# Kernel optimization log

Measured on AMD Instinct MI355X. Metric: run time of the kernel, lower is better.

## Reference

```python
import jax, jax.numpy as jnp
import numpy as np

BLOCKS, LAYERS, KS = 4, 2, 2
DILATIONS = [2 ** i for _ in range(BLOCKS) for i in range(LAYERS)]  # [1,2]*4
B, C_IN, N, T = 16, 2, 2048, 12
RC, DC, SC, EC, OUT = 32, 32, 256, 512, 12
L = BLOCKS * LAYERS
BN_EPS = 1e-5


def setup_inputs() -> dict:
    key = jax.random.key(0)
    ks = jax.random.split(key, 24)
    # raw inputs
    x = jax.random.normal(ks[0], (B, C_IN, N, T), dtype=jnp.float32)
    # two fixed supports: row-normalized random adjacency (dense, as in GraphWaveNet transition matrices)
    A_raw = jax.random.uniform(ks[1], (2, N, N), dtype=jnp.float32)
    A = A_raw / jnp.sum(A_raw, axis=2, keepdims=True)
    nodevec1 = jax.random.normal(ks[2], (N, 10), dtype=jnp.float32)
    nodevec2 = jax.random.normal(ks[3], (10, N), dtype=jnp.float32)
    s = 0.1  # weight scale to keep activations in a sane range
    filter_w = jax.random.normal(ks[4], (L, DC, RC, KS), dtype=jnp.float32) * s
    filter_b = jax.random.normal(ks[5], (L, DC), dtype=jnp.float32) * s
    gate_w = jax.random.normal(ks[6], (L, DC, RC, KS), dtype=jnp.float32) * s
    gate_b = jax.random.normal(ks[7], (L, DC), dtype=jnp.float32) * s
    skip_w = jax.random.normal(ks[8], (L, SC, DC), dtype=jnp.float32) * s
    skip_b = jax.random.normal(ks[9], (L, SC), dtype=jnp.float32) * s
    gcn_w = jax.random.normal(ks[10], (L, RC, 7 * DC), dtype=jnp.float32) * s
    gcn_b = jax.random.normal(ks[11], (L, RC), dtype=jnp.float32) * s
    bn_gamma = 1.0 + 0.1 * jax.random.normal(ks[12], (L, RC), dtype=jnp.float32)
    bn_beta = 0.1 * jax.random.normal(ks[13], (L, RC), dtype=jnp.float32)
    bn_mean = 0.1 * jax.random.normal(ks[14], (L, RC), dtype=jnp.float32)
    bn_var = 1.0 + jax.random.uniform(ks[15], (L, RC), dtype=jnp.float32)
    start_w = jax.random.normal(ks[16], (RC, C_IN), dtype=jnp.float32) * s
    start_b = jax.random.normal(ks[17], (RC,), dtype=jnp.float32) * s
    end1_w = jax.random.normal(ks[18], (EC, SC), dtype=jnp.float32) * s
    end1_b = jax.random.normal(ks[19], (EC,), dtype=jnp.float32) * s
    end2_w = jax.random.normal(ks[20], (OUT, EC), dtype=jnp.float32) * s
    end2_b = jax.random.normal(ks[21], (OUT,), dtype=jnp.float32) * s
    return dict(x=x, A=A, nodevec1=nodevec1, nodevec2=nodevec2,
                filter_w=filter_w, filter_b=filter_b, gate_w=gate_w, gate_b=gate_b,
                skip_w=skip_w, skip_b=skip_b, gcn_w=gcn_w, gcn_b=gcn_b,
                bn_gamma=bn_gamma, bn_beta=bn_beta, bn_mean=bn_mean, bn_var=bn_var,
                start_w=start_w, start_b=start_b, end1_w=end1_w, end1_b=end1_b,
                end2_w=end2_w, end2_b=end2_b)


def _conv1x1(x, w, b):
    # x: [b,c,n,t], w: [o,c] -> [b,o,n,t]
    return jnp.einsum('oc,bcnt->bont', w, x) + b[None, :, None, None]


def _dilated_conv2(x, w, b, d):
    # kernel (1,2) with time dilation d; out length T-d (valid conv)
    xa, xb = x[..., :-d], x[..., d:]
    y = jnp.einsum('oc,bcnt->bont', w[:, :, 0], xa) + jnp.einsum('oc,bcnt->bont', w[:, :, 1], xb)
    return y + b[None, :, None, None]


def _fwd(x, A, nodevec1, nodevec2, filter_w, filter_b, gate_w, gate_b,
         skip_w, skip_b, gcn_w, gcn_b, bn_gamma, bn_beta, bn_mean, bn_var,
         start_w, start_b, end1_w, end1_b, end2_w, end2_b):
    # pad 1 step at the start of time; T becomes 13 == receptive_field
    x = jnp.pad(x, ((0, 0), (0, 0), (0, 0), (1, 0)))
    x = x[:, :2]
    x = _conv1x1(x, start_w, start_b)  # [B,RC,N,13]
    # adaptive adjacency
    adp = jax.nn.softmax(jax.nn.relu(nodevec1 @ nodevec2), axis=1)
    supports = [A[0], A[1], adp]
    skip = None
    for i, d in enumerate(DILATIONS):
        residual = x
        filt = jnp.tanh(_dilated_conv2(residual, filter_w[i], filter_b[i], d))
        gate = jax.nn.sigmoid(_dilated_conv2(residual, gate_w[i], gate_b[i], d))
        x = filt * gate  # [B,DC,N,T-d]
        s = _conv1x1(x, skip_w[i], skip_b[i])  # [B,SC,N,T']
        skip = s if skip is None else s + skip[..., -s.shape[3]:]
        # GCN: order-2 diffusion over 3 supports, concat, 1x1 mix (dropout is identity in eval)
        outs = [x]
        for a in supports:
            x1 = jnp.einsum('bcvt,vw->bcwt', x, a)
            x2 = jnp.einsum('bcvt,vw->bcwt', x1, a)
            outs.extend([x1, x2])
        h = jnp.concatenate(outs, axis=1)  # [B,7*DC,N,T']
        x = _conv1x1(h, gcn_w[i], gcn_b[i])
        x = x + residual[..., -x.shape[3]:]
        # BatchNorm2d in eval mode (running stats)
        inv = bn_gamma[i] / jnp.sqrt(bn_var[i] + BN_EPS)
        x = (x - bn_mean[i][None, :, None, None]) * inv[None, :, None, None] + bn_beta[i][None, :, None, None]
    x = jax.nn.relu(skip)
    x = jax.nn.relu(_conv1x1(x, end1_w, end1_b))
    x = _conv1x1(x, end2_w, end2_b)  # [B,OUT,N,1]
    return x


def reference(x, A, nodevec1, nodevec2, filter_w, filter_b, gate_w, gate_b,
              skip_w, skip_b, gcn_w, gcn_b, bn_gamma, bn_beta, bn_mean, bn_var,
              start_w, start_b, end1_w, end1_b, end2_w, end2_b):
    return _fwd(x, A, nodevec1, nodevec2, filter_w, filter_b, gate_w, gate_b,
                skip_w, skip_b, gcn_w, gcn_b, bn_gamma, bn_beta, bn_mean, bn_var,
                start_w, start_b, end1_w, end1_b, end2_w, end2_b)
```

## Files before the change

### kernel.cpp

```cpp
#include <hip/hip_runtime.h>
#include <math.h>


#define NNODE 2048
#define NLAYER 8
#define SSTR ((size_t)NNODE * NNODE)

typedef unsigned short u16;
typedef unsigned int u32;
typedef __attribute__((ext_vector_type(8))) short bf16x8;
typedef __attribute__((ext_vector_type(4))) float f32x4;

__device__ __forceinline__ u16 f2bf(float f) {
    unsigned u = __builtin_bit_cast(unsigned, f);
    u += 0x7fffu + ((u >> 16) & 1u);
    return (u16)(u >> 16);
}
__device__ __forceinline__ float bf2f(u16 h) {
    unsigned u = ((unsigned)h) << 16;
    return __builtin_bit_cast(float, u);
}
__device__ __forceinline__ float bflo(u32 p) { return __builtin_bit_cast(float, p << 16); }
__device__ __forceinline__ float bfhi(u32 p) { return __builtin_bit_cast(float, p & 0xffff0000u); }
__device__ __forceinline__ u32 pack2(float a, float b) {
    return (u32)f2bf(a) | ((u32)f2bf(b) << 16);
}

__device__ __forceinline__ void gld16(const void* g, void* l) {
    __builtin_amdgcn_global_load_lds(
        (const __attribute__((address_space(1))) unsigned int*)g,
        (__attribute__((address_space(3))) unsigned int*)l, 16, 0, 0);
}

__global__ __launch_bounds__(256) void k_adp_mm(const float* __restrict__ nv1,
                                                const float* __restrict__ nv2,
                                                float* __restrict__ P) {
    int v = blockIdx.y;
    int w = blockIdx.x * 256 + threadIdx.x;
    float acc = 0.f;
#pragma unroll
    for (int k = 0; k < 10; ++k) acc += nv1[v * 10 + k] * nv2[k * NNODE + w];
    P[(size_t)v * NNODE + w] = acc;
}

__global__ __launch_bounds__(256) void k_softmax(float* __restrict__ P) {
    int v = blockIdx.x, tid = threadIdx.x;
    float* row = P + (size_t)v * NNODE;
    float m = 0.f;
    for (int w = tid; w < NNODE; w += 256) m = fmaxf(m, fmaxf(row[w], 0.f));
#pragma unroll
    for (int off = 32; off > 0; off >>= 1) m = fmaxf(m, __shfl_down(m, off));
    __shared__ float redm[4];
    __shared__ float reds[4];
    int wave = tid >> 6, lane = tid & 63;
    if (lane == 0) redm[wave] = m;
    __syncthreads();
    m = fmaxf(fmaxf(redm[0], redm[1]), fmaxf(redm[2], redm[3]));
    float s = 0.f;
    for (int w = tid; w < NNODE; w += 256) s += expf(fmaxf(row[w], 0.f) - m);
#pragma unroll
    for (int off = 32; off > 0; off >>= 1) s += __shfl_down(s, off);
    if (lane == 0) reds[wave] = s;
    __syncthreads();
    s = reds[0] + reds[1] + reds[2] + reds[3];
    float inv = 1.f / s;
    for (int w = tid; w < NNODE; w += 256) row[w] = expf(fmaxf(row[w], 0.f) - m) * inv;
}

__global__ __launch_bounds__(256) void k_transp(const float* __restrict__ A,
                                                const float* __restrict__ adp,
                                                u16* __restrict__ ST,
                                                u16* __restrict__ Sbf) {
    __shared__ float tile[32][33];
    int s = blockIdx.z;
    const float* src = (s < 2) ? (A + (size_t)s * SSTR) : adp;
    int v0 = blockIdx.y * 32, w0 = blockIdx.x * 32;
    int tx = threadIdx.x & 31, ty = threadIdx.x >> 5;
    u16* dst2 = Sbf + (size_t)s * SSTR;
#pragma unroll
    for (int p = 0; p < 4; ++p) {
        float v = src[(size_t)(v0 + ty + p * 8) * NNODE + w0 + tx];
        tile[ty + p * 8][tx] = v;
        dst2[(size_t)(v0 + ty + p * 8) * NNODE + w0 + tx] = f2bf(v);
    }
    __syncthreads();
    u16* dst = ST + (size_t)(2 * s) * SSTR;
#pragma unroll
    for (int p = 0; p < 4; ++p)
        dst[(size_t)(w0 + ty + p * 8) * NNODE + v0 + tx] = f2bf(tile[tx][ty + p * 8]);
}

__global__ __launch_bounds__(256) void k_skprep(const float* __restrict__ skw,
                                                const float* __restrict__ skb,
                                                u16* __restrict__ skwB,
                                                float* __restrict__ skbsum) {
    int idx = blockIdx.x * 256 + threadIdx.x;
    int sc = idx >> 8, k = idx & 255, l = k >> 5, ci = k & 31;
    skwB[idx] = f2bf(skw[((size_t)l * 256 + sc) * 32 + ci]);
    if (blockIdx.x == 0) {
        float s = 0.f;
#pragma unroll
        for (int ll = 0; ll < 8; ++ll) s += skb[ll * 256 + threadIdx.x];
        skbsum[threadIdx.x] = s;
    }
}

__global__ __launch_bounds__(256) void k_gemm_mfma(
    const u16* __restrict__ A, int lda, size_t asstr,
    const u16* __restrict__ BT, size_t bsstr,
    u16* __restrict__ C, int ldc, size_t csstr, int sbase) {
    __shared__ u16 Asl[128 * 32];
    __shared__ u16 Bsl[128 * 32];
    const int tid = threadIdx.x;
    const int wave = tid >> 6, lane = tid & 63;
    const int sidx = sbase + blockIdx.z;
    const u16* Ab = A + sidx * asstr + (size_t)blockIdx.y * 128 * lda;
    const u16* Bb = BT + sidx * bsstr + (size_t)blockIdx.x * 128 * NNODE;
    const int tr = tid >> 2;
    const int tc = (tid & 3) * 8;
    char* AslB = (char*)Asl + wave * 1024;
    char* BslB = (char*)Bsl + wave * 1024;
    const int wm = (wave & 1) * 64, wn = (wave >> 1) * 64;
    const int fr = lane & 15;
    const int fk = (lane >> 4) * 8;
    f32x4 acc[4][4];
#pragma unroll
    for (int i = 0; i < 4; ++i)
#pragma unroll
        for (int j = 0; j < 4; ++j) acc[i][j] = (f32x4){0.f, 0.f, 0.f, 0.f};

    for (int k0 = 0; k0 < 2048; k0 += 32) {
        gld16(Ab + (size_t)tr * lda + k0 + tc, AslB);
        gld16(Ab + (size_t)(tr + 64) * lda + k0 + tc, AslB + 4096);
        gld16(Bb + (size_t)tr * NNODE + k0 + tc, BslB);
        gld16(Bb + (size_t)(tr + 64) * NNODE + k0 + tc, BslB + 4096);
        __syncthreads();
        bf16x8 af[4], bf[4];
#pragma unroll
        for (int i = 0; i < 4; ++i)
            af[i] = *(const bf16x8*)&Asl[(wm + i * 16 + fr) * 32 + fk];
#pragma unroll
        for (int j = 0; j < 4; ++j)
            bf[j] = *(const bf16x8*)&Bsl[(wn + j * 16 + fr) * 32 + fk];
#pragma unroll
        for (int i = 0; i < 4; ++i)
#pragma unroll
            for (int j = 0; j < 4; ++j)
                acc[i][j] = __builtin_amdgcn_mfma_f32_16x16x32_bf16(af[i], bf[j], acc[i][j], 0, 0, 0);
        __syncthreads();
    }
    u16* Cb = C + sidx * csstr + (size_t)(blockIdx.y * 128 + wm) * ldc + blockIdx.x * 128 + wn;
    const int orow = (lane >> 4) * 4;
#pragma unroll
    for (int i = 0; i < 4; ++i)
#pragma unroll
        for (int j = 0; j < 4; ++j)
#pragma unroll
            for (int r = 0; r < 4; ++r)
                Cb[(size_t)(i * 16 + orow + r) * ldc + j * 16 + fr] = f2bf(acc[i][j][r]);
}

__global__ __launch_bounds__(512, 2) void k_gemmZ(const u16* __restrict__ Xg,
                                                  const u16* __restrict__ ST,
                                                  u16* __restrict__ Z, int pass) {
    __shared__ __align__(16) char ldsb[131072];
    const int tid = threadIdx.x;
    const int wave = tid >> 6, lane = tid & 63;
    const int m0 = blockIdx.y * 256;
    const int slice = pass * 3 + (blockIdx.x >> 3);
    const int n0 = (blockIdx.x & 7) * 256;
    const u16* AbG = Xg + (size_t)m0 * 2048;
    const u16* BbG = ST + (size_t)slice * SSTR + (size_t)n0 * 2048;

    const int xorc = ((tid & 7) ^ ((tid >> 3) & 7)) << 3;
    const size_t aRow = (size_t)(tid >> 3) * 2048 + xorc;
    const int bRowLoc = ((tid >> 8) << 6) + (((tid >> 6) & 3) << 3) + ((tid >> 3) & 7);
    const size_t bRow = (size_t)bRowLoc * 2048 + xorc;
    const int aw = wave << 10;
    const int bw = ((wave >> 2) << 13) + ((wave & 3) << 10);

    const int fr = lane & 15;
    const int cl4 = lane >> 4;
    const int ch0 = (cl4 ^ (fr & 7)) << 4;
    const int ch1 = ch0 ^ 64;
    const int aRd = ((wave & 1) << 14) + fr * 128;
    const int bRd = ((wave >> 1) << 13) + fr * 128;
    const int wm = (wave & 1) << 7;
    const int wn = (wave >> 1) << 6;

    char* A0 = ldsb;
    char* A1 = ldsb + 32768;
    char* B0 = ldsb + 65536;
    char* B1 = ldsb + 98304;

    auto STA = [&](char* Abase, int k0, int q) {
        const size_t g = (size_t)(q << 6) * 2048 + aRow + k0;
        gld16(AbG + g, Abase + (q << 13) + aw);
        gld16(AbG + g + (size_t)128 * 2048, Abase + 16384 + (q << 13) + aw);
    };
    auto STB = [&](char* Bbase, int k0, int q) {
        const size_t g = (size_t)(q << 5) * 2048 + bRow + k0;
        gld16(BbG + g, Bbase + (q << 12) + bw);
        gld16(BbG + g + (size_t)128 * 2048, Bbase + 16384 + (q << 12) + bw);
    };

    f32x4 acc[8][4];
#pragma unroll
    for (int i = 0; i < 8; ++i)
#pragma unroll
        for (int j = 0; j < 4; ++j) acc[i][j] = (f32x4){0.f, 0.f, 0.f, 0.f};

    STA(A0, 0, 0); STA(A0, 0, 1); STB(B0, 0, 0); STB(B0, 0, 1);
    STA(A1, 64, 0); STB(B1, 64, 0); STB(B1, 64, 1);
    asm volatile("s_waitcnt vmcnt(6)" ::: "memory");
    asm volatile("s_barrier" ::: "memory");

    char *Ac = A0, *Ao = A1, *Bc = B0, *Bo = B1;
    bf16x8 af[4][2], bfl[2][2], bfh[2][2];

    for (int T = 0; T < 32; ++T) {
#pragma unroll
        for (int i = 0; i < 4; ++i) {
            af[i][0] = *(const bf16x8*)(Ac + aRd + (i << 11) + ch0);
            af[i][1] = *(const bf16x8*)(Ac + aRd + (i << 11) + ch1);
        }
#pragma unroll
        for (int j = 0; j < 2; ++j) {
            bfl[j][0] = *(const bf16x8*)(Bc + bRd + (j << 11) + ch0);
            bfl[j][1] = *(const bf16x8*)(Bc + bRd + (j << 11) + ch1);
        }
        if (T < 31) STA(Ao, (T + 1) * 64, 1);
        asm volatile("s_barrier" ::: "memory");
        asm volatile("s_waitcnt lgkmcnt(0)" ::: "memory");
        __builtin_amdgcn_sched_barrier(0);
        __builtin_amdgcn_s_setprio(1);
#pragma unroll
        for (int i = 0; i < 4; ++i)
#pragma unroll
            for (int j = 0; j < 2; ++j) {
                acc[i][j] = __builtin_amdgcn_mfma_f32_16x16x32_bf16(af[i][0], bfl[j][0], acc[i][j], 0, 0, 0);
                acc[i][j] = __builtin_amdgcn_mfma_f32_16x16x32_bf16(af[i][1], bfl[j][1], acc[i][j], 0, 0, 0);
            }
        __builtin_amdgcn_s_setprio(0);
#pragma unroll
        for (int j = 0; j < 2; ++j) {
            bfh[j][0] = *(const bf16x8*)(Bc + bRd + 4096 + (j << 11) + ch0);
            bfh[j][1] = *(const bf16x8*)(Bc + bRd + 4096 + (j << 11) + ch1);
        }
        asm volatile("s_barrier" ::: "memory");
        asm volatile("s_waitcnt lgkmcnt(0)" ::: "memory");
        __builtin_amdgcn_sched_barrier(0);
        __builtin_amdgcn_s_setprio(1);
#pragma unroll
        for (int i = 0; i < 4; ++i)
#pragma unroll
            for (int j = 0; j < 2; ++j) {
                acc[i][2 + j] = __builtin_amdgcn_mfma_f32_16x16x32_bf16(af[i][0], bfh[j][0], acc[i][2 + j], 0, 0, 0);
                acc[i][2 + j] = __builtin_amdgcn_mfma_f32_16x16x32_bf16(af[i][1], bfh[j][1], acc[i][2 + j], 0, 0, 0);
            }
        __builtin_amdgcn_s_setprio(0);
#pragma unroll
        for (int i = 0; i < 4; ++i) {
            af[i][0] = *(const bf16x8*)(Ac + aRd + 8192 + (i << 11) + ch0);
            af[i][1] = *(const bf16x8*)(Ac + aRd + 8192 + (i << 11) + ch1);
        }
        if (T < 30) { STA(Ac, (T + 2) * 64, 0); STB(Bc, (T + 2) * 64, 0); }
        asm volatile("s_barrier" ::: "memory");
        asm volatile("s_waitcnt lgkmcnt(0)" ::: "memory");
        __builtin_amdgcn_sched_barrier(0);
        __builtin_amdgcn_s_setprio(1);
#pragma unroll
        for (int i = 0; i < 4; ++i)
#pragma unroll
            for (int j = 0; j < 2; ++j) {
                acc[4 + i][2 + j] = __builtin_amdgcn_mfma_f32_16x16x32_bf16(af[i][0], bfh[j][0], acc[4 + i][2 + j], 0, 0, 0);
                acc[4 + i][2 + j] = __builtin_amdgcn_mfma_f32_16x16x32_bf16(af[i][1], bfh[j][1], acc[4 + i][2 + j], 0, 0, 0);
            }
        __builtin_amdgcn_s_setprio(0);
        if (T < 30) STB(Bc, (T + 2) * 64, 1);
        asm volatile("s_barrier" ::: "memory");
        __builtin_amdgcn_sched_barrier(0);
        __builtin_amdgcn_s_setprio(1);
#pragma unroll
        for (int i = 0; i < 4; ++i)
#pragma unroll
            for (int j = 0; j < 2; ++j) {
                acc[4 + i][j] = __builtin_amdgcn_mfma_f32_16x16x32_bf16(af[i][0], bfl[j][0], acc[4 + i][j], 0, 0, 0);
                acc[4 + i][j] = __builtin_amdgcn_mfma_f32_16x16x32_bf16(af[i][1], bfl[j][1], acc[4 + i][j], 0, 0, 0);
            }
        __builtin_amdgcn_s_setprio(0);
        if (T < 30) {
            asm volatile("s_waitcnt vmcnt(6)" ::: "memory");
        } else if (T == 30) {
            asm volatile("s_waitcnt vmcnt(0)" ::: "memory");
        }
        asm volatile("s_barrier" ::: "memory");
        char* t;
        t = Ac; Ac = Ao; Ao = t;
        t = Bc; Bc = Bo; Bo = t;
    }

    const int col0 = (blockIdx.x >> 3) * 2048 + (blockIdx.x & 7) * 256;
    u16* Cb = Z + (size_t)(m0 + wm) * 6144 + col0 + wn;
    const int orow = cl4 * 4;
#pragma unroll
    for (int i = 0; i < 8; ++i)
#pragma unroll
        for (int j = 0; j < 4; ++j)
#pragma unroll
            for (int r = 0; r < 4; ++r)
                Cb[(size_t)(i * 16 + orow + r) * 6144 + j * 16 + fr] = f2bf(acc[i][j][r]);
}

__global__ __launch_bounds__(256) void k_gemmZ128(const u16* __restrict__ Xg,
                                                  const u16* __restrict__ ST,
                                                  u16* __restrict__ Z, int pass) {
    __shared__ u16 Asl[2][128 * 32];
    __shared__ u16 Bsl[2][128 * 32];
    const int tid = threadIdx.x;
    const int wave = tid >> 6, lane = tid & 63;
    const int m0 = blockIdx.y * 128;
    const int slice = pass * 3 + (blockIdx.x >> 4);
    const int nIn = (blockIdx.x & 15) * 128;
    const u16* Ab = Xg + (size_t)m0 * 2048;
    const u16* Bb = ST + (size_t)slice * SSTR + (size_t)nIn * NNODE;
    const int tr = tid >> 2;
    const int tc = (tid & 3) * 8;
    char* AslB0 = (char*)Asl[0] + wave * 1024;
    char* AslB1 = (char*)Asl[1] + wave * 1024;
    char* BslB0 = (char*)Bsl[0] + wave * 1024;
    char* BslB1 = (char*)Bsl[1] + wave * 1024;
    const int wm = (wave & 1) * 64, wn = (wave >> 1) * 64;
    const int fr = lane & 15;
    const int fk = (lane >> 4) * 8;
    f32x4 acc[4][4];
#pragma unroll
    for (int i = 0; i < 4; ++i)
#pragma unroll
        for (int j = 0; j < 4; ++j) acc[i][j] = (f32x4){0.f, 0.f, 0.f, 0.f};

    for (int k0 = 0; k0 < 2048; k0 += 64) {
        gld16(Ab + (size_t)tr * 2048 + k0 + tc, AslB0);
        gld16(Ab + (size_t)(tr + 64) * 2048 + k0 + tc, AslB0 + 4096);
        gld16(Ab + (size_t)tr * 2048 + k0 + 32 + tc, AslB1);
        gld16(Ab + (size_t)(tr + 64) * 2048 + k0 + 32 + tc, AslB1 + 4096);
        gld16(Bb + (size_t)tr * NNODE + k0 + tc, BslB0);
        gld16(Bb + (size_t)(tr + 64) * NNODE + k0 + tc, BslB0 + 4096);
        gld16(Bb + (size_t)tr * NNODE + k0 + 32 + tc, BslB1);
        gld16(Bb + (size_t)(tr + 64) * NNODE + k0 + 32 + tc, BslB1 + 4096);
        __syncthreads();
#pragma unroll
        for (int h = 0; h < 2; ++h) {
            bf16x8 af[4], bf[4];
#pragma unroll
            for (int i = 0; i < 4; ++i)
                af[i] = *(const bf16x8*)&Asl[h][(wm + i * 16 + fr) * 32 + fk];
#pragma unroll
            for (int j = 0; j < 4; ++j)
                bf[j] = *(const bf16x8*)&Bsl[h][(wn + j * 16 + fr) * 32 + fk];
#pragma unroll
            for (int i = 0; i < 4; ++i)
#pragma unroll
                for (int j = 0; j < 4; ++j)
                    acc[i][j] = __builtin_amdgcn_mfma_f32_16x16x32_bf16(af[i], bf[j], acc[i][j], 0, 0, 0);
        }
        __syncthreads();
    }
    u16* Cb = Z + (size_t)(m0 + wm) * 6144 + blockIdx.x * 128 + wn;
    const int orow = (lane >> 4) * 4;
#pragma unroll
    for (int i = 0; i < 4; ++i)
#pragma unroll
        for (int j = 0; j < 4; ++j)
#pragma unroll
            for (int r = 0; r < 4; ++r)
                Cb[(size_t)(i * 16 + orow + r) * 6144 + j * 16 + fr] = f2bf(acc[i][j][r]);
}

__global__ __launch_bounds__(256) void k_start(const float* __restrict__ xin,
                                               const float* __restrict__ sw,
                                               const float* __restrict__ sb,
                                               u16* __restrict__ out, int b0) {
    int n = blockIdx.x * 256 + threadIdx.x;
    int t = blockIdx.y;
    int bl = blockIdx.z;
    int b = b0 + bl;
    float x0 = 0.f, x1 = 0.f;
    if (t > 0) {
        x0 = xin[((size_t)(b * 2 + 0) * NNODE + n) * 12 + (t - 1)];
        x1 = xin[((size_t)(b * 2 + 1) * NNODE + n) * 12 + (t - 1)];
    }
#pragma unroll
    for (int co = 0; co < 32; ++co) {
        float v = sw[co * 2 + 0] * x0 + sw[co * 2 + 1] * x1 + sb[co];
        out[((size_t)(bl * 32 + co) * 13 + t) * NNODE + n] = f2bf(v);
    }
}

__global__ __launch_bounds__(256) void k_gate(const u16* __restrict__ cur,
                                              u16* __restrict__ xg,
                                              u16* __restrict__ nxt,
                                              int T, int Tn, int d,
                                              const float* __restrict__ fw,
                                              const float* __restrict__ fb,
                                              const float* __restrict__ gw,
                                              const float* __restrict__ gb,
                                              const float* __restrict__ gcwl,
                                              const float* __restrict__ gcbl,
                                              u16* __restrict__ xl,
                                              int layer, int donxt) {
    __shared__ float4 wp[1024];
    __shared__ float w0[32][33];
    int tid = threadIdx.x;
#pragma unroll
    for (int u = 0; u < 4; ++u) {
        int idx = tid + u * 256;
        int ci = idx >> 5, co = idx & 31;
        wp[idx] = make_float4(fw[co * 64 + ci * 2], fw[co * 64 + ci * 2 + 1],
                              gw[co * 64 + ci * 2], gw[co * 64 + ci * 2 + 1]);
        w0[ci][co] = gcwl[co * 224 + ci];
    }
    __syncthreads();
    int n = blockIdx.x * 512 + tid * 2;
    int t = blockIdx.y;
    int bl = blockIdx.z;
    float f0[32], f1[32], g0[32], g1[32];
#pragma unroll
    for (int co = 0; co < 32; ++co) { f0[co] = 0.f; f1[co] = 0.f; g0[co] = 0.f; g1[co] = 0.f; }
    for (int ci = 0; ci < 32; ++ci) {
        size_t ba = ((size_t)(bl * 32 + ci) * T + t) * NNODE + n;
        size_t bb = ((size_t)(bl * 32 + ci) * T + t + d) * NNODE + n;
        u32 ua = *(const u32*)&cur[ba];
        u32 ub = *(const u32*)&cur[bb];
        float xa0 = bflo(ua), xa1 = bfhi(ua);
        float xb0 = bflo(ub), xb1 = bfhi(ub);
#pragma unroll
        for (int co = 0; co < 32; ++co) {
            float4 w = wp[ci * 32 + co];
            f0[co] += w.x * xa0 + w.y * xb0;
            f1[co] += w.x * xa1 + w.y * xb1;
            g0[co] += w.z * xa0 + w.w * xb0;
            g1[co] += w.z * xa1 + w.w * xb1;
        }
    }
#pragma unroll
    for (int co = 0; co < 32; ++co) {
        float fbv = fb[co], gbv = gb[co];
        float a0 = tanhf(f0[co] + fbv) * (1.f / (1.f + expf(-(g0[co] + gbv))));
        float a1 = tanhf(f1[co] + fbv) * (1.f / (1.f + expf(-(g1[co] + gbv))));
        f0[co] = a0; f1[co] = a1;
        size_t o = ((size_t)(bl * 32 + co) * Tn + t) * NNODE + n;
        *(u32*)&xg[o] = pack2(a0, a1);
    }
    if (t == Tn - 1) {
        size_t o2 = ((size_t)(bl * 2048 + n)) * 256 + layer * 32;
#pragma unroll
        for (int co = 0; co < 32; ++co) {
            xl[o2 + co] = f2bf(f0[co]);
            xl[o2 + 256 + co] = f2bf(f1[co]);
        }
    }
    if (donxt) {
#pragma unroll
        for (int cop = 0; cop < 32; ++cop) {
            float s0 = gcbl[cop], s1 = s0;
#pragma unroll
            for (int ci = 0; ci < 32; ++ci) {
                float wv = w0[ci][cop];
                s0 += wv * f0[ci];
                s1 += wv * f1[ci];
            }
            size_t o = ((size_t)(bl * 32 + cop) * Tn + t) * NNODE + n;
            *(u32*)&nxt[o] = pack2(s0, s1);
        }
    }
}

__global__ __launch_bounds__(256) void k_accum(const u16* __restrict__ Z,
                                               int cbase,
                                               const float* __restrict__ gcnw,
                                               u16* __restrict__ outp,
                                               const u16* __restrict__ resid,
                                               int Tn, int d, int finalf,
                                               const float* __restrict__ bng,
                                               const float* __restrict__ bnb,
                                               const float* __restrict__ bnm,
                                               const float* __restrict__ bnv) {
    __shared__ float wl[3][32][32];
    int tid = threadIdx.x;
    for (int u = tid; u < 3072; u += 256) {
        int g = u >> 10, ci = (u >> 5) & 31, co = u & 31;
        wl[g][ci][co] = gcnw[co * 224 + cbase + g * 32 + ci];
    }
    __syncthreads();
    int n = blockIdx.x * 512 + tid * 2;
    int t = blockIdx.y, bl = blockIdx.z;
    float a0[32], a1[32];
#pragma unroll
    for (int co = 0; co < 32; ++co) { a0[co] = 0.f; a1[co] = 0.f; }
    for (int ci = 0; ci < 32; ++ci) {
        size_t m = (size_t)(bl * 32 + ci) * Tn + t;
#pragma unroll
        for (int g = 0; g < 3; ++g) {
            u32 zz = *(const u32*)&Z[m * 6144 + g * 2048 + n];
            float v0 = bflo(zz), v1 = bfhi(zz);
#pragma unroll
            for (int cq = 0; cq < 8; ++cq) {
                float4 w = *(const float4*)&wl[g][ci][cq * 4];
                a0[cq * 4 + 0] += w.x * v0; a1[cq * 4 + 0] += w.x * v1;
                a0[cq * 4 + 1] += w.y * v0; a1[cq * 4 + 1] += w.y * v1;
                a0[cq * 4 + 2] += w.z * v0; a1[cq * 4 + 2] += w.z * v1;
                a0[cq * 4 + 3] += w.w * v0; a1[cq * 4 + 3] += w.w * v1;
            }
        }
    }
#pragma unroll
    for (int co = 0; co < 32; ++co) {
        size_t o = ((size_t)(bl * 32 + co) * Tn + t) * NNODE + n;
        u32 oo = *(const u32*)&outp[o];
        float v0 = bflo(oo) + a0[co];
        float v1 = bfhi(oo) + a1[co];
        if (finalf) {
            size_t ro = ((size_t)(bl * 32 + co) * (Tn + d) + t + d) * NNODE + n;
            u32 rr = *(const u32*)&resid[ro];
            v0 += bflo(rr); v1 += bfhi(rr);
            float inv = bng[co] * rsqrtf(bnv[co] + 1e-5f);
            float mu = bnm[co], be = bnb[co];
            v0 = (v0 - mu) * inv + be;
            v1 = (v1 - mu) * inv + be;
        }
        *(u32*)&outp[o] = pack2(v0, v1);
    }
}

__global__ __launch_bounds__(256) void k_cast(const float* __restrict__ src,
                                              u16* __restrict__ dst) {
    int i = blockIdx.x * 256 + threadIdx.x;
    dst[i] = f2bf(src[i]);
}

__global__ __launch_bounds__(256) void k_skipg(const u16* __restrict__ xl,
                                               const u16* __restrict__ skwB,
                                               const float* __restrict__ skbsum,
                                               u16* __restrict__ skipT) {
    __shared__ u16 Asl[128 * 32];
    __shared__ u16 Bsl[128 * 32];
    const int tid = threadIdx.x;
    const int wave = tid >> 6, lane = tid & 63;
    const int m0 = blockIdx.y * 128;
    const int n0 = blockIdx.x * 128;
    const int tr = tid >> 2;
    const int tc = (tid & 3) * 8;
    char* AslB = (char*)Asl + wave * 1024;
    char* BslB = (char*)Bsl + wave * 1024;
    const int wm = (wave & 1) * 64, wn = (wave >> 1) * 64;
    const int fr = lane & 15;
    const int fk = (lane >> 4) * 8;
    const u16* Ab = xl + (size_t)m0 * 256;
    const u16* Bb = skwB + (size_t)n0 * 256;
    f32x4 acc[4][4];
#pragma unroll
    for (int i = 0; i < 4; ++i)
#pragma unroll
        for (int j = 0; j < 4; ++j) acc[i][j] = (f32x4){0.f, 0.f, 0.f, 0.f};
    for (int k0 = 0; k0 < 256; k0 += 32) {
        gld16(Ab + (size_t)tr * 256 + k0 + tc, AslB);
        gld16(Ab + (size_t)(tr + 64) * 256 + k0 + tc, AslB + 4096);
        gld16(Bb + (size_t)tr * 256 + k0 + tc, BslB);
        gld16(Bb + (size_t)(tr + 64) * 256 + k0 + tc, BslB + 4096);
        __syncthreads();
        bf16x8 af[4], bf[4];
#pragma unroll
        for (int i = 0; i < 4; ++i)
            af[i] = *(const bf16x8*)&Asl[(wm + i * 16 + fr) * 32 + fk];
#pragma unroll
        for (int j = 0; j < 4; ++j)
            bf[j] = *(const bf16x8*)&Bsl[(wn + j * 16 + fr) * 32 + fk];
#pragma unroll
        for (int i = 0; i < 4; ++i)
#pragma unroll
            for (int j = 0; j < 4; ++j)
                acc[i][j] = __builtin_amdgcn_mfma_f32_16x16x32_bf16(af[i], bf[j], acc[i][j], 0, 0, 0);
        __syncthreads();
    }
    const int orow = (lane >> 4) * 4;
#pragma unroll
    for (int i = 0; i < 4; ++i)
#pragma unroll
        for (int r = 0; r < 4; ++r) {
            int m = m0 + wm + i * 16 + orow + r;
            size_t ob = (size_t)m * 256 + n0 + wn;
#pragma unroll
            for (int j = 0; j < 4; ++j) {
                int col = n0 + wn + j * 16 + fr;
                skipT[ob + j * 16 + fr] = f2bf(fmaxf(acc[i][j][r] + skbsum[col], 0.f));
            }
        }
}

__global__ __launch_bounds__(256) void k_end1m(const u16* __restrict__ E1,
                                               const u16* __restrict__ skT,
                                               const float* __restrict__ bias,
                                               u16* __restrict__ h) {
    __shared__ u16 Asl[128 * 32];
    __shared__ u16 Bsl[128 * 32];
    const int tid = threadIdx.x;
    const int wave = tid >> 6, lane = tid & 63;
    const int b = blockIdx.z;
    const int m0 = blockIdx.y * 128;
    const int n0 = blockIdx.x * 128;
    const int tr = tid >> 2;
    const int tc = (tid & 3) * 8;
    char* AslB = (char*)Asl + wave * 1024;
    char* BslB = (char*)Bsl + wave * 1024;
    const int wm = (wave & 1) * 64, wn = (wave >> 1) * 64;
    const int fr = lane & 15;
    const int fk = (lane >> 4) * 8;
    const u16* Ab = E1 + (size_t)m0 * 256;
    const u16* Bb = skT + ((size_t)b * NNODE + n0) * 256;
    f32x4 acc[4][4];
#pragma unroll
    for (int i = 0; i < 4; ++i)
#pragma unroll
        for (int j = 0; j < 4; ++j) acc[i][j] = (f32x4){0.f, 0.f, 0.f, 0.f};
    for (int k0 = 0; k0 < 256; k0 += 32) {
        gld16(Ab + (size_t)tr * 256 + k0 + tc, AslB);
        gld16(Ab + (size_t)(tr + 64) * 256 + k0 + tc, AslB + 4096);
        gld16(Bb + (size_t)tr * 256 + k0 + tc, BslB);
        gld16(Bb + (size_t)(tr + 64) * 256 + k0 + tc, BslB + 4096);
        __syncthreads();
        bf16x8 af[4], bf[4];
#pragma unroll
        for (int i = 0; i < 4; ++i)
            af[i] = *(const bf16x8*)&Asl[(wm + i * 16 + fr) * 32 + fk];
#pragma unroll
        for (int j = 0; j < 4; ++j)
            bf[j] = *(const bf16x8*)&Bsl[(wn + j * 16 + fr) * 32 + fk];
#pragma unroll
        for (int i = 0; i < 4; ++i)
#pragma unroll
            for (int j = 0; j < 4; ++j)
                acc[i][j] = __builtin_amdgcn_mfma_f32_16x16x32_bf16(af[i], bf[j], acc[i][j], 0, 0, 0);
        __syncthreads();
    }
    const int orow = (lane >> 4) * 4;
#pragma unroll
    for (int i = 0; i < 4; ++i)
#pragma unroll
        for (int r = 0; r < 4; ++r) {
            int m = m0 + wm + i * 16 + orow + r;
            float bs = bias[m];
            size_t ob = ((size_t)b * 512 + m) * NNODE + n0 + wn;
#pragma unroll
            for (int j = 0; j < 4; ++j)
                h[ob + j * 16 + fr] = f2bf(fmaxf(acc[i][j][r] + bs, 0.f));
        }
}

__global__ __launch_bounds__(256) void k_end2(const u16* __restrict__ h,
                                              const float* __restrict__ w,
                                              const float* __restrict__ bias,
                                              float* __restrict__ out) {
    __shared__ float wl[12][512];
    int tid = threadIdx.x;
    for (int u = tid; u < 6144; u += 256) wl[u >> 9][u & 511] = w[u];
    __syncthreads();
    int n = blockIdx.x * 256 + tid;
    int b = blockIdx.y;
    float acc[12];
#pragma unroll
    for (int o = 0; o < 12; ++o) acc[o] = 0.f;
#pragma unroll 4
    for (int e = 0; e < 512; ++e) {
        float v = bf2f(h[((size_t)(b * 512) + e) * NNODE + n]);
#pragma unroll
        for (int o = 0; o < 12; ++o) acc[o] += wl[o][e] * v;
    }
#pragma unroll
    for (int o = 0; o < 12; ++o)
        out[((size_t)(b * 12) + o) * NNODE + n] = acc[o] + bias[o];
}

extern "C" void kernel_launch(void* const* d_in, const int* in_sizes, int n_in,
                              void* d_out, int out_size, void* d_ws, size_t ws_size,
                              hipStream_t stream) {
    const float* x_in = (const float*)d_in[0];
    const float* A    = (const float*)d_in[1];
    const float* nv1  = (const float*)d_in[2];
    const float* nv2  = (const float*)d_in[3];
    const float* fw   = (const float*)d_in[4];
    const float* fb   = (const float*)d_in[5];
    const float* gw   = (const float*)d_in[6];
    const float* gb   = (const float*)d_in[7];
    const float* skw  = (const float*)d_in[8];
    const float* skb  = (const float*)d_in[9];
    const float* gcw  = (const float*)d_in[10];
    const float* gcb  = (const float*)d_in[11];
    const float* bng  = (const float*)d_in[12];
    const float* bnb  = (const float*)d_in[13];
    const float* bnm  = (const float*)d_in[14];
    const float* bnv  = (const float*)d_in[15];
    const float* stw  = (const float*)d_in[16];
    const float* stb  = (const float*)d_in[17];
    const float* e1w  = (const float*)d_in[18];
    const float* e1b  = (const float*)d_in[19];
    const float* e2w  = (const float*)d_in[20];
    const float* e2b  = (const float*)d_in[21];
    (void)in_sizes; (void)n_in; (void)out_size;

    const int BL = (ws_size >= 239075328UL) ? 16 : 8;
    const int nch = 16 / BL;
    const size_t bufsz = (size_t)BL * 1703936UL;

    char* base = (char*)d_ws;
    u16*   ST     = (u16*)base;
    u16*   xlast  = (u16*)(base + 50331648UL);
    u16*   skwB   = (u16*)(base + 67108864UL);
    float* skbsum = (float*)(base + 67239936UL);
    u16*   bufA = (u16*)(base + 83886080UL);
    u16*   bufB = (u16*)(base + 83886080UL + bufsz);
    u16*   xg   = (u16*)(base + 83886080UL + 2 * bufsz);
    u16*   Z    = (u16*)(base + 83886080UL + 2 * bufsz + (size_t)BL * 1572864UL);
    float* adp  = (float*)Z;
    u16*   Sbf  = (u16*)bufA;
    u16*   h     = (u16*)(base + 83886080UL);
    u16*   skipT = (u16*)(base + 83886080UL + 33554432UL);
    u16*   E1bf  = (u16*)ST;

    k_adp_mm<<<dim3(8, 2048), 256, 0, stream>>>(nv1, nv2, adp);
    k_skprep<<<256, 256, 0, stream>>>(skw, skb, skwB, skbsum);
    k_softmax<<<2048, 256, 0, stream>>>(adp);
    k_transp<<<dim3(64, 64, 3), 256, 0, stream>>>(A, adp, ST, Sbf);
    k_gemm_mfma<<<dim3(16, 16, 3), 256, 0, stream>>>(
        ST, NNODE, 2 * SSTR, Sbf, SSTR, ST + SSTR, NNODE, 2 * SSTR, 0);

    static const int DIL[NLAYER] = {1, 2, 1, 2, 1, 2, 1, 2};
    for (int ch = 0; ch < nch; ++ch) {
        int b0 = ch * BL;
        k_start<<<dim3(8, 13, BL), 256, 0, stream>>>(x_in, stw, stb, bufA, b0);
        u16* cur = bufA;
        u16* nxt = bufB;
        int T = 13;
        for (int i = 0; i < NLAYER; ++i) {
            int d = DIL[i], Tn = T - d;
            int last = (i == NLAYER - 1);
            k_gate<<<dim3(4, Tn, BL), 256, 0, stream>>>(cur, xg, nxt, T, Tn, d,
                fw + i * 2048, fb + i * 32, gw + i * 2048, gb + i * 32,
                gcw + i * 32 * 224, gcb + i * 32,
                xlast + (size_t)b0 * 2048 * 256, i, last ? 0 : 1);
            if (last) break;
            const float* gcwi = gcw + i * 32 * 224;
            if (Tn == 6 || Tn == 3) {
                for (int p = 0; p < 2; ++p) {
                    k_gemmZ128<<<dim3(48, BL * Tn / 4), 256, 0, stream>>>(xg, ST, Z, p);
                    k_accum<<<dim3(4, Tn, BL), 256, 0, stream>>>(
                        Z, 32 + 96 * p, gcwi, nxt, cur, Tn, d, p,
                        bng + i * 32, bnb + i * 32, bnm + i * 32, bnv + i * 32);
                }
            } else {
                for (int p = 0; p < 2; ++p) {
                    k_gemmZ<<<dim3(24, BL * 32 * Tn / 256), 512, 0, stream>>>(xg, ST, Z, p);
                    k_accum<<<dim3(4, Tn, BL), 256, 0, stream>>>(
                        Z, 32 + 96 * p, gcwi, nxt, cur, Tn, d, p,
                        bng + i * 32, bnb + i * 32, bnm + i * 32, bnv + i * 32);
                }
            }
            u16* tmp = cur; cur = nxt; nxt = tmp;
            T = Tn;
        }
    }
    k_cast<<<512, 256, 0, stream>>>(e1w, E1bf);
    k_skipg<<<dim3(2, 256), 256, 0, stream>>>(xlast, skwB, skbsum, skipT);
    k_end1m<<<dim3(16, 4, 16), 256, 0, stream>>>(E1bf, skipT, e1b, h);
    k_end2<<<dim3(8, 16), 256, 0, stream>>>(h, e2w, e2b, (float*)d_out);
}
```

Measured before the change: 2.985 ms.

## Use pipelined 256x256 GEMM for support squaring and merge accumulation passes

Replaces the simple 128x128 MFMA GEMM that computes the squared support matrices with a 512-thread, double-buffered, XOR-swizzled 256x256 kernel, modelled on the existing k_gemmZ with interleaved barriers and priority hints. It also adds k_accum2, which consumes both Z passes in one kernel when the workspace allows. This removes a second read-modify-write of the output and the residual/BN epilogue. The merged path needs twice the Z buffer and is only used when BL==16 and Tn is small enough or the workspace is large enough.

```diff
diff --git a/kernel.cpp b/kernel.cpp
--- a/kernel.cpp
+++ b/kernel.cpp
@@ -105,59 +105,154 @@
     }
 }
 
-__global__ __launch_bounds__(256) void k_gemm_mfma(
-    const u16* __restrict__ A, int lda, size_t asstr,
-    const u16* __restrict__ BT, size_t bsstr,
-    u16* __restrict__ C, int ldc, size_t csstr, int sbase) {
-    __shared__ u16 Asl[128 * 32];
-    __shared__ u16 Bsl[128 * 32];
+__global__ __launch_bounds__(512, 2) void k_gemmS(const u16* __restrict__ ST,
+                                                  const u16* __restrict__ Sbf) {
+    __shared__ __align__(16) char ldsb[131072];
     const int tid = threadIdx.x;
     const int wave = tid >> 6, lane = tid & 63;
-    const int sidx = sbase + blockIdx.z;
-    const u16* Ab = A + sidx * asstr + (size_t)blockIdx.y * 128 * lda;
-    const u16* Bb = BT + sidx * bsstr + (size_t)blockIdx.x * 128 * NNODE;
-    const int tr = tid >> 2;
-    const int tc = (tid & 3) * 8;
-    char* AslB = (char*)Asl + wave * 1024;
-    char* BslB = (char*)Bsl + wave * 1024;
-    const int wm = (wave & 1) * 64, wn = (wave >> 1) * 64;
+    const int m0 = blockIdx.y * 256;
+    const int slice = blockIdx.x >> 3;
+    const int n0 = (blockIdx.x & 7) * 256;
+    const u16* AbG = ST + (size_t)(2 * slice) * SSTR + (size_t)m0 * 2048;
+    const u16* BbG = Sbf + (size_t)slice * SSTR + (size_t)n0 * 2048;
+
+    const int xorc = ((tid & 7) ^ ((tid >> 3) & 7)) << 3;
+    const size_t aRow = (size_t)(tid >> 3) * 2048 + xorc;
+    const int bRowLoc = ((tid >> 8) << 6) + (((tid >> 6) & 3) << 3) + ((tid >> 3) & 7);
+    const size_t bRow = (size_t)bRowLoc * 2048 + xorc;
+    const int aw = wave << 10;
+    const int bw = ((wave >> 2) << 13) + ((wave & 3) << 10);
+
     const int fr = lane & 15;
-    const int fk = (lane >> 4) * 8;
-    f32x4 acc[4][4];
-#pragma unroll
-    for (int i = 0; i < 4; ++i)
+    const int cl4 = lane >> 4;
+    const int ch0 = (cl4 ^ (fr & 7)) << 4;
+    const int ch1 = ch0 ^ 64;
+    const int aRd = ((wave & 1) << 14) + fr * 128;
+    const int bRd = ((wave >> 1) << 13) + fr * 128;
+    const int wm = (wave & 1) << 7;
+    const int wn = (wave >> 1) << 6;
+
+    char* A0 = ldsb;
+    char* A1 = ldsb + 32768;
+    char* B0 = ldsb + 65536;
+    char* B1 = ldsb + 98304;
+
+    auto STA = [&](char* Abase, int k0, int q) {
+        const size_t g = (size_t)(q << 6) * 2048 + aRow + k0;
+        gld16(AbG + g, Abase + (q << 13) + aw);
+        gld16(AbG + g + (size_t)128 * 2048, Abase + 16384 + (q << 13) + aw);
+    };
+    auto STB = [&](char* Bbase, int k0, int q) {
+        const size_t g = (size_t)(q << 5) * 2048 + bRow + k0;
+        gld16(BbG + g, Bbase + (q << 12) + bw);
+        gld16(BbG + g + (size_t)128 * 2048, Bbase + 16384 + (q << 12) + bw);
+    };
+
+    f32x4 acc[8][4];
+#pragma unroll
+    for (int i = 0; i < 8; ++i)
 #pragma unroll
         for (int j = 0; j < 4; ++j) acc[i][j] = (f32x4){0.f, 0.f, 0.f, 0.f};
 
-    for (int k0 = 0; k0 < 2048; k0 += 32) {
-        gld16(Ab + (size_t)tr * lda + k0 + tc, AslB);
-        gld16(Ab + (size_t)(tr + 64) * lda + k0 + tc, AslB + 4096);
-        gld16(Bb + (size_t)tr * NNODE + k0 + tc, BslB);
-        gld16(Bb + (size_t)(tr + 64) * NNODE + k0 + tc, BslB + 4096);
-        __syncthreads();
-        bf16x8 af[4], bf[4];
-#pragma unroll
-        for (int i = 0; i < 4; ++i)
-            af[i] = *(const bf16x8*)&Asl[(wm + i * 16 + fr) * 32 + fk];
+    STA(A0, 0, 0); STA(A0, 0, 1); STB(B0, 0, 0); STB(B0, 0, 1);
+    STA(A1, 64, 0); STB(B1, 64, 0); STB(B1, 64, 1);
+    asm volatile("s_waitcnt vmcnt(6)" ::: "memory");
+    asm volatile("s_barrier" ::: "memory");
+
+    char *Ac = A0, *Ao = A1, *Bc = B0, *Bo = B1;
+    bf16x8 af[4][2], bfl[2][2], bfh[2][2];
+
+    for (int T = 0; T < 32; ++T) {
+#pragma unroll
+        for (int i = 0; i < 4; ++i) {
+            af[i][0] = *(const bf16x8*)(Ac + aRd + (i << 11) + ch0);
+            af[i][1] = *(const bf16x8*)(Ac + aRd + (i << 11) + ch1);
+        }
+#pragma unroll
+        for (int j = 0; j < 2; ++j) {
+            bfl[j][0] = *(const bf16x8*)(Bc + bRd + (j << 11) + ch0);
+            bfl[j][1] = *(const bf16x8*)(Bc + bRd + (j << 11) + ch1);
+        }
+        if (T < 31) STA(Ao, (T + 1) * 64, 1);
+        asm volatile("s_barrier" ::: "memory");
+        asm volatile("s_waitcnt lgkmcnt(0)" ::: "memory");
+        __builtin_amdgcn_sched_barrier(0);
+        __builtin_amdgcn_s_setprio(1);
+#pragma unroll
+        for (int i = 0; i < 4; ++i)
+#pragma unroll
+            for (int j = 0; j < 2; ++j) {
+                acc[i][j] = __builtin_amdgcn_mfma_f32_16x16x32_bf16(af[i][0], bfl[j][0], acc[i][j], 0, 0, 0);
+                acc[i][j] = __builtin_amdgcn_mfma_f32_16x16x32_bf16(af[i][1], bfl[j][1], acc[i][j], 0, 0, 0);
+            }
+        __builtin_amdgcn_s_setprio(0);
+#pragma unroll
+        for (int j = 0; j < 2; ++j) {
+            bfh[j][0] = *(const bf16x8*)(Bc + bRd + 4096 + (j << 11) + ch0);
+            bfh[j][1] = *(const bf16x8*)(Bc + bRd + 4096 + (j << 11) + ch1);
+        }
+        asm volatile("s_barrier" ::: "memory");
+        asm volatile("s_waitcnt lgkmcnt(0)" ::: "memory");
+        __builtin_amdgcn_sched_barrier(0);
+        __builtin_amdgcn_s_setprio(1);
+#pragma unroll
+        for (int i = 0; i < 4; ++i)
+#pragma unroll
+            for (int j = 0; j < 2; ++j) {
+                acc[i][2 + j] = __builtin_amdgcn_mfma_f32_16x16x32_bf16(af[i][0], bfh[j][0], acc[i][2 + j], 0, 0, 0);
+                acc[i][2 + j] = __builtin_amdgcn_mfma_f32_16x16x32_bf16(af[i][1], bfh[j][1], acc[i][2 + j], 0, 0, 0);
+            }
+        __builtin_amdgcn_s_setprio(0);
+#pragma unroll
+        for (int i = 0; i < 4; ++i) {
+            af[i][0] = *(const bf16x8*)(Ac + aRd + 8192 + (i << 11) + ch0);
+            af[i][1] = *(const bf16x8*)(Ac + aRd + 8192 + (i << 11) + ch1);
+        }
+        if (T < 30) { STA(Ac, (T + 2) * 64, 0); STB(Bc, (T + 2) * 64, 0); }
+        asm volatile("s_barrier" ::: "memory");
+        asm volatile("s_waitcnt lgkmcnt(0)" ::: "memory");
+        __builtin_amdgcn_sched_barrier(0);
+        __builtin_amdgcn_s_setprio(1);
+#pragma unroll
+        for (int i = 0; i < 4; ++i)
+#pragma unroll
+            for (int j = 0; j < 2; ++j) {
+                acc[4 + i][2 + j] = __builtin_amdgcn_mfma_f32_16x16x32_bf16(af[i][0], bfh[j][0], acc[4 + i][2 + j], 0, 0, 0);
+                acc[4 + i][2 + j] = __builtin_amdgcn_mfma_f32_16x16x32_bf16(af[i][1], bfh[j][1], acc[4 + i][2 + j], 0, 0, 0);
+            }
+        __builtin_amdgcn_s_setprio(0);
+        if (T < 30) STB(Bc, (T + 2) * 64, 1);
+        asm volatile("s_barrier" ::: "memory");
+        __builtin_amdgcn_sched_barrier(0);
+        __builtin_amdgcn_s_setprio(1);
+#pragma unroll
+        for (int i = 0; i < 4; ++i)
+#pragma unroll
+            for (int j = 0; j < 2; ++j) {
+                acc[4 + i][j] = __builtin_amdgcn_mfma_f32_16x16x32_bf16(af[i][0], bfl[j][0], acc[4 + i][j], 0, 0, 0);
+                acc[4 + i][j] = __builtin_amdgcn_mfma_f32_16x16x32_bf16(af[i][1], bfl[j][1], acc[4 + i][j], 0, 0, 0);
+            }
+        __builtin_amdgcn_s_setprio(0);
+        if (T < 30) {
+            asm volatile("s_waitcnt vmcnt(6)" ::: "memory");
+        } else if (T == 30) {
+            asm volatile("s_waitcnt vmcnt(0)" ::: "memory");
+        }
+        asm volatile("s_barrier" ::: "memory");
+        char* t;
+        t = Ac; Ac = Ao; Ao = t;
+        t = Bc; Bc = Bo; Bo = t;
+    }
+
+    u16* Cb = (u16*)ST + (size_t)(2 * slice + 1) * SSTR + (size_t)(m0 + wm) * 2048 + n0 + wn;
+    const int orow = cl4 * 4;
+#pragma unroll
+    for (int i = 0; i < 8; ++i)
 #pragma unroll
         for (int j = 0; j < 4; ++j)
-            bf[j] = *(const bf16x8*)&Bsl[(wn + j * 16 + fr) * 32 + fk];
-#pragma unroll
-        for (int i = 0; i < 4; ++i)
-#pragma unroll
-            for (int j = 0; j < 4; ++j)
-                acc[i][j] = __builtin_amdgcn_mfma_f32_16x16x32_bf16(af[i], bf[j], acc[i][j], 0, 0, 0);
-        __syncthreads();
-    }
-    u16* Cb = C + sidx * csstr + (size_t)(blockIdx.y * 128 + wm) * ldc + blockIdx.x * 128 + wn;
-    const int orow = (lane >> 4) * 4;
-#pragma unroll
-    for (int i = 0; i < 4; ++i)
-#pragma unroll
-        for (int j = 0; j < 4; ++j)
 #pragma unroll
             for (int r = 0; r < 4; ++r)
-                Cb[(size_t)(i * 16 + orow + r) * ldc + j * 16 + fr] = f2bf(acc[i][j][r]);
+                Cb[(size_t)(i * 16 + orow + r) * 2048 + j * 16 + fr] = f2bf(acc[i][j][r]);
 }
 
 __global__ __launch_bounds__(512, 2) void k_gemmZ(const u16* __restrict__ Xg,
@@ -529,6 +624,64 @@
             v0 = (v0 - mu) * inv + be;
             v1 = (v1 - mu) * inv + be;
         }
+        *(u32*)&outp[o] = pack2(v0, v1);
+    }
+}
+
+__global__ __launch_bounds__(256) void k_accum2(const u16* __restrict__ Z0,
+                                                const u16* __restrict__ Z1,
+                                                const float* __restrict__ gcnw,
+                                                u16* __restrict__ outp,
+                                                const u16* __restrict__ resid,
+                                                int Tn, int d,
+                                                const float* __restrict__ bng,
+                                                const float* __restrict__ bnb,
+                                                const float* __restrict__ bnm,
+                                                const float* __restrict__ bnv) {
+    __shared__ float wl[6][32][32];
+    int tid = threadIdx.x;
+    for (int u = tid; u < 6144; u += 256) {
+        int pg = u >> 10, ci = (u >> 5) & 31, co = u & 31;
+        int cbase = (pg < 3) ? (32 + pg * 32) : (128 + (pg - 3) * 32);
+        wl[pg][ci][co] = gcnw[co * 224 + cbase + ci];
+    }
+    __syncthreads();
+    int n = blockIdx.x * 512 + tid * 2;
+    int t = blockIdx.y, bl = blockIdx.z;
+    float a0[32], a1[32];
+#pragma unroll
+    for (int co = 0; co < 32; ++co) { a0[co] = 0.f; a1[co] = 0.f; }
+    for (int ci = 0; ci < 32; ++ci) {
+        size_t m = (size_t)(bl * 32 + ci) * Tn + t;
+#pragma unroll
+        for (int pg = 0; pg < 6; ++pg) {
+            const u16* Zs = (pg < 3) ? Z0 : Z1;
+            int g = (pg < 3) ? pg : pg - 3;
+            u32 zz = *(const u32*)&Zs[m * 6144 + g * 2048 + n];
+            float v0 = bflo(zz), v1 = bfhi(zz);
+#pragma unroll
+            for (int cq = 0; cq < 8; ++cq) {
+                float4 w = *(const float4*)&wl[pg][ci][cq * 4];
+                a0[cq * 4 + 0] += w.x * v0; a1[cq * 4 + 0] += w.x * v1;
+                a0[cq * 4 + 1] += w.y * v0; a1[cq * 4 + 1] += w.y * v1;
+                a0[cq * 4 + 2] += w.z * v0; a1[cq * 4 + 2] += w.z * v1;
+                a0[cq * 4 + 3] += w.w * v0; a1[cq * 4 + 3] += w.w * v1;
+            }
+        }
+    }
+#pragma unroll
+    for (int co = 0; co < 32; ++co) {
+        size_t o = ((size_t)(bl * 32 + co) * Tn + t) * NNODE + n;
+        u32 oo = *(const u32*)&outp[o];
+        float v0 = bflo(oo) + a0[co];
+        float v1 = bfhi(oo) + a1[co];
+        size_t ro = ((size_t)(bl * 32 + co) * (Tn + d) + t + d) * NNODE + n;
+        u32 rr = *(const u32*)&resid[ro];
+        v0 += bflo(rr); v1 += bfhi(rr);
+        float inv = bng[co] * rsqrtf(bnv[co] + 1e-5f);
+        float mu = bnm[co], be = bnb[co];
+        v0 = (v0 - mu) * inv + be;
+        v1 = (v1 - mu) * inv + be;
         *(u32*)&outp[o] = pack2(v0, v1);
     }
 }
@@ -731,8 +884,7 @@
     k_skprep<<<256, 256, 0, stream>>>(skw, skb, skwB, skbsum);
     k_softmax<<<2048, 256, 0, stream>>>(adp);
     k_transp<<<dim3(64, 64, 3), 256, 0, stream>>>(A, adp, ST, Sbf);
-    k_gemm_mfma<<<dim3(16, 16, 3), 256, 0, stream>>>(
-        ST, NNODE, 2 * SSTR, Sbf, SSTR, ST + SSTR, NNODE, 2 * SSTR, 0);
+    k_gemmS<<<dim3(24, 8), 512, 0, stream>>>(ST, Sbf);
 
     static const int DIL[NLAYER] = {1, 2, 1, 2, 1, 2, 1, 2};
     for (int ch = 0; ch < nch; ++ch) {
@@ -750,13 +902,30 @@
                 xlast + (size_t)b0 * 2048 * 256, i, last ? 0 : 1);
             if (last) break;
             const float* gcwi = gcw + i * 32 * 224;
+            const size_t Msz = (size_t)BL * 32 * Tn * 6144;
+            const bool canMerge =
+                (BL == 16) && (Tn <= 6 || (Tn == 7 && ws_size >= 251658240UL));
             if (Tn == 6 || Tn == 3) {
-                for (int p = 0; p < 2; ++p) {
-                    k_gemmZ128<<<dim3(48, BL * Tn / 4), 256, 0, stream>>>(xg, ST, Z, p);
-                    k_accum<<<dim3(4, Tn, BL), 256, 0, stream>>>(
-                        Z, 32 + 96 * p, gcwi, nxt, cur, Tn, d, p,
+                if (canMerge) {
+                    k_gemmZ128<<<dim3(48, BL * Tn / 4), 256, 0, stream>>>(xg, ST, Z, 0);
+                    k_gemmZ128<<<dim3(48, BL * Tn / 4), 256, 0, stream>>>(xg, ST, Z + Msz, 1);
+                    k_accum2<<<dim3(4, Tn, BL), 256, 0, stream>>>(
+                        Z, Z + Msz, gcwi, nxt, cur, Tn, d,
                         bng + i * 32, bnb + i * 32, bnm + i * 32, bnv + i * 32);
+                } else {
+                    for (int p = 0; p < 2; ++p) {
+                        k_gemmZ128<<<dim3(48, BL * Tn / 4), 256, 0, stream>>>(xg, ST, Z, p);
+                        k_accum<<<dim3(4, Tn, BL), 256, 0, stream>>>(
+                            Z, 32 + 96 * p, gcwi, nxt, cur, Tn, d, p,
+                            bng + i * 32, bnb + i * 32, bnm + i * 32, bnv + i * 32);
+                    }
                 }
+            } else if (canMerge) {
+                k_gemmZ<<<dim3(24, BL * 32 * Tn / 256), 512, 0, stream>>>(xg, ST, Z, 0);
+                k_gemmZ<<<dim3(24, BL * 32 * Tn / 256), 512, 0, stream>>>(xg, ST, Z + Msz, 1);
+                k_accum2<<<dim3(4, Tn, BL), 256, 0, stream>>>(
+                    Z, Z + Msz, gcwi, nxt, cur, Tn, d,
+                    bng + i * 32, bnb + i * 32, bnm + i * 32, bnv + i * 32);
             } else {
                 for (int p = 0; p < 2; ++p) {
                     k_gemmZ<<<dim3(24, BL * 32 * Tn / 256), 512, 0, stream>>>(xg, ST, Z, p);
```

New measurement: 2.917 ms. -2.3%, faster.
